# Kernel optimization log

Hardware: AMD Instinct MI355X
Metric: run time of the kernel (lower is better)

## Reference

```python
import jax, jax.numpy as jnp
import numpy as np

_EPS = 1e-06


def setup_inputs() -> dict:
    key = jax.random.key(0)
    k1, k2, k3, k4, k5 = jax.random.split(key, 5)
    B, N = 2, 8192
    return {
        "kp_before": jax.random.normal(k1, (B, N, 3), dtype=jnp.float32),
        "kp_warped_pred": jax.random.normal(k2, (B, N, 3), dtype=jnp.float32),
        "pose_gt": jax.random.normal(k3, (B, 3, 4), dtype=jnp.float32),
        "overlap_weights": jax.random.uniform(k4, (B, N), dtype=jnp.float32),
        "inlier_logits": jax.random.normal(k5, (B, N), dtype=jnp.float32),
    }


def _bce_with_logits(x, z):
    # elementwise BCEWithLogits: z*softplus(-x) + (1-z)*softplus(x)
    return z * jax.nn.softplus(-x) + (1.0 - z) * jax.nn.softplus(x)


def _balanced_loss(logits, label):
    # BalancedLoss: mean BCE within each of the 2 label groups, averaged over groups
    bce = _bce_with_logits(logits, label)
    loss = jnp.float32(0.0)
    for i in range(2):
        mask = (label == i).astype(jnp.float32)
        cnt = jnp.sum(mask)
        group = jnp.where(cnt > 0, jnp.sum(bce * mask) / jnp.maximum(cnt, 1.0), 0.0)
        loss = loss + group / 2.0
    return loss


def reference(kp_before, kp_warped_pred, pose_gt, overlap_weights, inlier_logits):
    B, N, _ = kp_before.shape
    M = B * N
    # se3_transform_list: warped_gt[b] = kp_before[b] @ R[b]^T + t[b]
    R = pose_gt[:, :, :3]            # [B,3,3]
    t = pose_gt[:, :, 3]             # [B,3]
    kp_warped_gt = jnp.einsum('bij,bnj->bni', R, kp_before) + t[:, None, :]
    # torch.cat(list, dim=0) over equal-sized chunks == reshape
    pred = kp_warped_pred.reshape(M, 3)
    gt = kp_warped_gt.reshape(M, 3)
    corr_err = pred - gt               # [M,3]
    # pairwise L2 distance matrix [M,M] (O(N^2) traffic) + 1-NN argmin
    sq = (jnp.sum(pred * pred, axis=1)[:, None]
          + jnp.sum(gt * gt, axis=1)[None, :]
          - 2.0 * (pred @ gt.T))
    dist_map = jnp.sqrt(jnp.maximum(sq, 0.0))
    knn_ind = jnp.argmin(dist_map, axis=1)
    binary_mask = (knn_ind == jnp.arange(M)).astype(jnp.float32)
    inlier_err = _balanced_loss(inlier_logits.reshape(M), binary_mask)
    # metric == 'mae'
    err = jnp.sum(jnp.abs(corr_err), axis=-1)  # [M]
    w = overlap_weights.reshape(M)
    mean_err = jnp.sum(w * err) / jnp.maximum(jnp.sum(w), _EPS)
    return mean_err + inlier_err
```

## Files before the change

### kernel.cpp

```cpp
#include <hip/hip_runtime.h>
#include <cstdint>

#define TPB 256
#define K_PRE 256
#define NSLICE 16

__global__ void __launch_bounds__(TPB) fused_prep_prefix(
        const float* __restrict__ kp_before,
        const float* __restrict__ pred,
        const float* __restrict__ pose,
        float4* __restrict__ gt4,
        float* __restrict__ thr,
        unsigned int* __restrict__ good,
        float* __restrict__ accum,
        int M, int N) {
    __shared__ float4 shg[K_PRE];
    int tid = threadIdx.x;
    int i = blockIdx.x * TPB + tid;

    if (blockIdx.x == 0 && tid < 8) accum[tid] = 0.0f;

    float sp = 0.f, tp0 = 0.f, tp1 = 0.f, tp2 = 0.f, dii = 0.f;
    if (i < M) {
        int b = i / N;
        const float* P = pose + b * 12;
        float k0 = kp_before[3*i+0];
        float k1 = kp_before[3*i+1];
        float k2 = kp_before[3*i+2];
        float g0 = fmaf(P[2],  k2, fmaf(P[1], k1, P[0]*k0)) + P[3];
        float g1 = fmaf(P[6],  k2, fmaf(P[5], k1, P[4]*k0)) + P[7];
        float g2 = fmaf(P[10], k2, fmaf(P[9], k1, P[8]*k0)) + P[11];
        float sg;
        {
            #pragma clang fp contract(off)
            sg = (g0*g0 + g1*g1) + g2*g2;
        }
        gt4[i] = make_float4(g0, g1, g2, sg);

        float p0 = pred[3*i+0], p1 = pred[3*i+1], p2 = pred[3*i+2];
        {
            #pragma clang fp contract(off)
            sp = (p0*p0 + p1*p1) + p2*p2;
        }
        tp0 = 2.0f*p0; tp1 = 2.0f*p1; tp2 = 2.0f*p2;
        float dot2 = fmaf(tp2, g2, fmaf(tp1, g1, tp0*g0));
        float v = (sp + sg) - dot2;
        dii = fmaxf(v, 0.0f);
        thr[i] = dii;
    }

    if (tid < K_PRE && tid < M) {
        int jp = tid;
        const float* Pj = pose + (jp / N) * 12;
        float q0 = kp_before[3*jp+0];
        float q1 = kp_before[3*jp+1];
        float q2 = kp_before[3*jp+2];
        float h0 = fmaf(Pj[2],  q2, fmaf(Pj[1], q1, Pj[0]*q0)) + Pj[3];
        float h1 = fmaf(Pj[6],  q2, fmaf(Pj[5], q1, Pj[4]*q0)) + Pj[7];
        float h2 = fmaf(Pj[10], q2, fmaf(Pj[9], q1, Pj[8]*q0)) + Pj[11];
        float hh;
        {
            #pragma clang fp contract(off)
            hh = (h0*h0 + h1*h1) + h2*h2;
        }
        shg[jp] = make_float4(h0, h1, h2, hh);
    }
    __syncthreads();

    if (i >= M) return;

    bool bad;
    if (i >= K_PRE) {
        float mn = __uint_as_float(0x7f7fffffu);
        for (int j = 0; j < K_PRE; j++) {
            float4 g = shg[j];
            float v = (sp + g.w) -
                      fmaf(tp2, g.z, fmaf(tp1, g.y, tp0 * g.x));
            mn = fminf(mn, v);
        }
        bad = (fmaxf(mn, 0.0f) <= dii);
    } else {
        float mnl = __uint_as_float(0x7f7fffffu);
        float mnr = __uint_as_float(0x7f7fffffu);
        for (int j = 0; j < i; j++) {
            float4 g = shg[j];
            float v = (sp + g.w) -
                      fmaf(tp2, g.z, fmaf(tp1, g.y, tp0 * g.x));
            mnl = fminf(mnl, v);
        }
        for (int j = i + 1; j < K_PRE; j++) {
            float4 g = shg[j];
            float v = (sp + g.w) -
                      fmaf(tp2, g.z, fmaf(tp1, g.y, tp0 * g.x));
            mnr = fminf(mnr, v);
        }
        bad = (fmaxf(mnl, 0.0f) <= dii) || (fmaxf(mnr, 0.0f) < dii);
    }
    good[i] = bad ? 0u : 1u;
}

__global__ void __launch_bounds__(TPB) suffix_kernel(
        const float* __restrict__ pred,
        const float4* __restrict__ gt4,
        const float* __restrict__ thr,
        unsigned int* __restrict__ good,
        int M) {
    __shared__ int cands[TPB];
    __shared__ int ncand;
    int s  = blockIdx.x & (NSLICE - 1);
    int r0 = (blockIdx.x / NSLICE) * TPB;
    if (threadIdx.x == 0) ncand = 0;
    __syncthreads();
    int i = r0 + threadIdx.x;
    if (i < M && good[i] == 1u) {
        int p = atomicAdd(&ncand, 1);
        cands[p] = i;
    }
    __syncthreads();
    int nc = ncand;
    if (nc == 0) return;

    int total = M - K_PRE;
    int per = (total + NSLICE - 1) / NSLICE;
    int js = K_PRE + s * per;
    int je = js + per; if (je > M) je = M;

    for (int e = 0; e < nc; e++) {
        int r = cands[e];
        float p0 = pred[3*r+0], p1 = pred[3*r+1], p2 = pred[3*r+2];
        float sp;
        {
            #pragma clang fp contract(off)
            sp = (p0*p0 + p1*p1) + p2*p2;
        }
        float tp0 = 2.0f*p0, tp1 = 2.0f*p1, tp2 = 2.0f*p2;
        float dii = thr[r];
        bool h = false;
        for (int j = js + threadIdx.x; j < je; j += TPB) {
            float4 g = gt4[j];
            float v = (sp + g.w) -
                      fmaf(tp2, g.z, fmaf(tp1, g.y, tp0 * g.x));
            float c = fmaxf(v, 0.0f);
            h = h || (c < dii && j != r) || (c == dii && j < r);
        }
        if (h) good[r] = 0u;
    }
}

__device__ inline float wave_red(float v) {
    #pragma unroll
    for (int off = 32; off > 0; off >>= 1) v += __shfl_down(v, off, 64);
    return v;
}

__global__ void __launch_bounds__(TPB) finalize_kernel(
        const float* __restrict__ pred,
        const float4* __restrict__ gt4,
        const float* __restrict__ ow,
        const float* __restrict__ logits,
        const unsigned int* __restrict__ good,
        float* __restrict__ accum,
        float* __restrict__ out,
        int M) {
    float werr = 0.f, wsum = 0.f, b1 = 0.f, c1 = 0.f, b0 = 0.f, c0 = 0.f;
    int stride = gridDim.x * blockDim.x;
    for (int i = blockIdx.x * blockDim.x + threadIdx.x; i < M; i += stride) {
        float x = logits[i];
        float l1p = log1pf(expf(-fabsf(x)));
        if (good[i] == 1u) {
            b1 += fmaxf(-x, 0.f) + l1p; c1 += 1.f;
        } else {
            b0 += fmaxf(x, 0.f) + l1p;  c0 += 1.f;
        }
        float4 g = gt4[i];
        float p0 = pred[3*i+0], p1 = pred[3*i+1], p2 = pred[3*i+2];
        float e = (fabsf(p0 - g.x) + fabsf(p1 - g.y)) + fabsf(p2 - g.z);
        float wi = ow[i];
        werr += wi * e;
        wsum += wi;
    }
    werr = wave_red(werr); wsum = wave_red(wsum);
    b1 = wave_red(b1); c1 = wave_red(c1);
    b0 = wave_red(b0); c0 = wave_red(c0);
    if ((threadIdx.x & 63) == 0) {
        atomicAdd(&accum[0], werr);
        atomicAdd(&accum[1], wsum);
        atomicAdd(&accum[2], b1);
        atomicAdd(&accum[3], c1);
        atomicAdd(&accum[4], b0);
        atomicAdd(&accum[5], c0);
    }
    __threadfence();
    __syncthreads();
    if (threadIdx.x == 0) {
        unsigned int* ctr = (unsigned int*)&accum[7];
        unsigned int old = atomicAdd(ctr, 1u);
        if (old == gridDim.x - 1) {
            float a0 = atomicAdd(&accum[0], 0.f);
            float a1 = atomicAdd(&accum[1], 0.f);
            float a2 = atomicAdd(&accum[2], 0.f);
            float a3 = atomicAdd(&accum[3], 0.f);
            float a4 = atomicAdd(&accum[4], 0.f);
            float a5 = atomicAdd(&accum[5], 0.f);
            float mean_err = a0 / fmaxf(a1, 1e-6f);
            float g1v = (a3 > 0.f) ? (a2 / fmaxf(a3, 1.f)) : 0.f;
            float g0v = (a5 > 0.f) ? (a4 / fmaxf(a5, 1.f)) : 0.f;
            out[0] = mean_err + (g0v * 0.5f + g1v * 0.5f);
        }
    }
}

extern "C" void kernel_launch(void* const* d_in, const int* in_sizes, int n_in,
                              void* d_out, int out_size, void* d_ws, size_t ws_size,
                              hipStream_t stream) {
    const float* kp_before = (const float*)d_in[0];
    const float* pred      = (const float*)d_in[1];
    const float* pose      = (const float*)d_in[2];
    const float* ow        = (const float*)d_in[3];
    const float* logits    = (const float*)d_in[4];
    float* out = (float*)d_out;

    int M = in_sizes[3];
    int B = in_sizes[2] / 12;
    int N = M / B;

    char* ws = (char*)d_ws;
    float4* gt4 = (float4*)ws;
    float* thr = (float*)(ws + (size_t)M * 16);
    unsigned int* good = (unsigned int*)(ws + (size_t)M * 20);
    float* accum = (float*)(ws + (size_t)M * 24);

    int nrb = (M + TPB - 1) / TPB;

    hipLaunchKernelGGL(fused_prep_prefix, dim3(nrb), dim3(TPB), 0, stream,
                       kp_before, pred, pose, gt4, thr, good, accum, M, N);

    hipLaunchKernelGGL(suffix_kernel, dim3(nrb * NSLICE), dim3(TPB), 0, stream,
                       pred, gt4, thr, good, M);

    hipLaunchKernelGGL(finalize_kernel, dim3(64), dim3(TPB), 0, stream,
                       pred, gt4, ow, logits, good, accum, out, M);
}
```

Measured before the change: 115.4 us.

## Prefilter against both batch prefixes and fuse suffix resolve with finalize

The shared-memory prefilter now checks each row against the first 256 gt points of both batch halves instead of only the first 256 overall, which is meant to reject more non-nearest candidates early. The separate sliced suffix kernel and the finalize kernel are merged. Each block now resolves its own surviving candidates by scanning the remaining columns itself and then reduces the loss terms directly. This saves one launch and the global good-array rewrite, but the per-candidate scan is no longer split across 16 slices, so blocks with many candidates do serial full-length scans and parallelism may drop.

```diff
diff --git a/kernel.cpp b/kernel.cpp
--- a/kernel.cpp
+++ b/kernel.cpp
@@ -2,8 +2,7 @@
 #include <cstdint>
 
 #define TPB 256
-#define K_PRE 256
-#define NSLICE 16
+#define PRE_PB 256
 
 __global__ void __launch_bounds__(TPB) fused_prep_prefix(
         const float* __restrict__ kp_before,
@@ -14,7 +13,7 @@
         unsigned int* __restrict__ good,
         float* __restrict__ accum,
         int M, int N) {
-    __shared__ float4 shg[K_PRE];
+    __shared__ float4 shg[2 * PRE_PB];
     int tid = threadIdx.x;
     int i = blockIdx.x * TPB + tid;
 
@@ -49,8 +48,10 @@
         thr[i] = dii;
     }
 
-    if (tid < K_PRE && tid < M) {
-        int jp = tid;
+    #pragma unroll
+    for (int half = 0; half < 2; half++) {
+        int jp = (half == 0) ? tid : (N + tid);
+        if (jp >= M) jp = tid;
         const float* Pj = pose + (jp / N) * 12;
         float q0 = kp_before[3*jp+0];
         float q1 = kp_before[3*jp+1];
@@ -63,67 +64,86 @@
             #pragma clang fp contract(off)
             hh = (h0*h0 + h1*h1) + h2*h2;
         }
-        shg[jp] = make_float4(h0, h1, h2, hh);
+        shg[half * PRE_PB + tid] = make_float4(h0, h1, h2, hh);
     }
     __syncthreads();
 
     if (i >= M) return;
 
     bool bad;
-    if (i >= K_PRE) {
+    bool cleanB = (i >= PRE_PB) && (i < N);
+    bool cleanA = (i >= N + PRE_PB);
+    if (cleanA) {
         float mn = __uint_as_float(0x7f7fffffu);
-        for (int j = 0; j < K_PRE; j++) {
-            float4 g = shg[j];
+        for (int k = 0; k < 2 * PRE_PB; k++) {
+            float4 g = shg[k];
             float v = (sp + g.w) -
                       fmaf(tp2, g.z, fmaf(tp1, g.y, tp0 * g.x));
             mn = fminf(mn, v);
         }
         bad = (fmaxf(mn, 0.0f) <= dii);
-    } else {
+    } else if (cleanB) {
         float mnl = __uint_as_float(0x7f7fffffu);
         float mnr = __uint_as_float(0x7f7fffffu);
-        for (int j = 0; j < i; j++) {
-            float4 g = shg[j];
+        for (int k = 0; k < PRE_PB; k++) {
+            float4 g = shg[k];
             float v = (sp + g.w) -
                       fmaf(tp2, g.z, fmaf(tp1, g.y, tp0 * g.x));
             mnl = fminf(mnl, v);
         }
-        for (int j = i + 1; j < K_PRE; j++) {
-            float4 g = shg[j];
+        for (int k = PRE_PB; k < 2 * PRE_PB; k++) {
+            float4 g = shg[k];
             float v = (sp + g.w) -
                       fmaf(tp2, g.z, fmaf(tp1, g.y, tp0 * g.x));
             mnr = fminf(mnr, v);
         }
         bad = (fmaxf(mnl, 0.0f) <= dii) || (fmaxf(mnr, 0.0f) < dii);
+    } else {
+        bool h = false;
+        for (int k = 0; k < 2 * PRE_PB; k++) {
+            int j = (k < PRE_PB) ? k : (N + k - PRE_PB);
+            if (j >= M) j = k - PRE_PB;
+            float4 g = shg[k];
+            float v = (sp + g.w) -
+                      fmaf(tp2, g.z, fmaf(tp1, g.y, tp0 * g.x));
+            float c = fmaxf(v, 0.0f);
+            h = h || (c < dii && j != i) || (c == dii && j < i);
+        }
+        bad = h;
     }
     good[i] = bad ? 0u : 1u;
 }
 
-__global__ void __launch_bounds__(TPB) suffix_kernel(
+__device__ inline float wave_red(float v) {
+    #pragma unroll
+    for (int off = 32; off > 0; off >>= 1) v += __shfl_down(v, off, 64);
+    return v;
+}
+
+__global__ void __launch_bounds__(TPB) resolve_finalize(
         const float* __restrict__ pred,
         const float4* __restrict__ gt4,
         const float* __restrict__ thr,
-        unsigned int* __restrict__ good,
-        int M) {
+        const unsigned int* __restrict__ good,
+        const float* __restrict__ ow,
+        const float* __restrict__ logits,
+        float* __restrict__ accum,
+        float* __restrict__ out,
+        int M, int N) {
     __shared__ int cands[TPB];
     __shared__ int ncand;
-    int s  = blockIdx.x & (NSLICE - 1);
-    int r0 = (blockIdx.x / NSLICE) * TPB;
-    if (threadIdx.x == 0) ncand = 0;
-    __syncthreads();
-    int i = r0 + threadIdx.x;
-    if (i < M && good[i] == 1u) {
-        int p = atomicAdd(&ncand, 1);
-        cands[p] = i;
-    }
+    __shared__ unsigned char verd[TPB];
+    int tid = threadIdx.x;
+    int r0 = blockIdx.x * TPB;
+    int i = r0 + tid;
+
+    if (tid == 0) ncand = 0;
+    __syncthreads();
+    unsigned int gi = (i < M) ? good[i] : 0u;
+    verd[tid] = (unsigned char)gi;
+    if (i < M && gi) { int p = atomicAdd(&ncand, 1); cands[p] = i; }
     __syncthreads();
     int nc = ncand;
-    if (nc == 0) return;
-
-    int total = M - K_PRE;
-    int per = (total + NSLICE - 1) / NSLICE;
-    int js = K_PRE + s * per;
-    int je = js + per; if (je > M) je = M;
 
     for (int e = 0; e < nc; e++) {
         int r = cands[e];
@@ -136,53 +156,44 @@
         float tp0 = 2.0f*p0, tp1 = 2.0f*p1, tp2 = 2.0f*p2;
         float dii = thr[r];
         bool h = false;
-        for (int j = js + threadIdx.x; j < je; j += TPB) {
+        for (int j = PRE_PB + tid; j < N; j += TPB) {
             float4 g = gt4[j];
             float v = (sp + g.w) -
                       fmaf(tp2, g.z, fmaf(tp1, g.y, tp0 * g.x));
             float c = fmaxf(v, 0.0f);
             h = h || (c < dii && j != r) || (c == dii && j < r);
         }
-        if (h) good[r] = 0u;
-    }
-}
-
-__device__ inline float wave_red(float v) {
-    #pragma unroll
-    for (int off = 32; off > 0; off >>= 1) v += __shfl_down(v, off, 64);
-    return v;
-}
-
-__global__ void __launch_bounds__(TPB) finalize_kernel(
-        const float* __restrict__ pred,
-        const float4* __restrict__ gt4,
-        const float* __restrict__ ow,
-        const float* __restrict__ logits,
-        const unsigned int* __restrict__ good,
-        float* __restrict__ accum,
-        float* __restrict__ out,
-        int M) {
+        for (int j = N + PRE_PB + tid; j < M; j += TPB) {
+            float4 g = gt4[j];
+            float v = (sp + g.w) -
+                      fmaf(tp2, g.z, fmaf(tp1, g.y, tp0 * g.x));
+            float c = fmaxf(v, 0.0f);
+            h = h || (c < dii && j != r) || (c == dii && j < r);
+        }
+        if (h) verd[r - r0] = 0;
+    }
+    __syncthreads();
+
     float werr = 0.f, wsum = 0.f, b1 = 0.f, c1 = 0.f, b0 = 0.f, c0 = 0.f;
-    int stride = gridDim.x * blockDim.x;
-    for (int i = blockIdx.x * blockDim.x + threadIdx.x; i < M; i += stride) {
+    if (i < M) {
         float x = logits[i];
         float l1p = log1pf(expf(-fabsf(x)));
-        if (good[i] == 1u) {
-            b1 += fmaxf(-x, 0.f) + l1p; c1 += 1.f;
+        if (verd[tid]) {
+            b1 = fmaxf(-x, 0.f) + l1p; c1 = 1.f;
         } else {
-            b0 += fmaxf(x, 0.f) + l1p;  c0 += 1.f;
+            b0 = fmaxf(x, 0.f) + l1p;  c0 = 1.f;
         }
         float4 g = gt4[i];
         float p0 = pred[3*i+0], p1 = pred[3*i+1], p2 = pred[3*i+2];
         float e = (fabsf(p0 - g.x) + fabsf(p1 - g.y)) + fabsf(p2 - g.z);
         float wi = ow[i];
-        werr += wi * e;
-        wsum += wi;
+        werr = wi * e;
+        wsum = wi;
     }
     werr = wave_red(werr); wsum = wave_red(wsum);
     b1 = wave_red(b1); c1 = wave_red(c1);
     b0 = wave_red(b0); c0 = wave_red(c0);
-    if ((threadIdx.x & 63) == 0) {
+    if ((tid & 63) == 0) {
         atomicAdd(&accum[0], werr);
         atomicAdd(&accum[1], wsum);
         atomicAdd(&accum[2], b1);
@@ -192,7 +203,7 @@
     }
     __threadfence();
     __syncthreads();
-    if (threadIdx.x == 0) {
+    if (tid == 0) {
         unsigned int* ctr = (unsigned int*)&accum[7];
         unsigned int old = atomicAdd(ctr, 1u);
         if (old == gridDim.x - 1) {
@@ -235,9 +246,6 @@
     hipLaunchKernelGGL(fused_prep_prefix, dim3(nrb), dim3(TPB), 0, stream,
                        kp_before, pred, pose, gt4, thr, good, accum, M, N);
 
-    hipLaunchKernelGGL(suffix_kernel, dim3(nrb * NSLICE), dim3(TPB), 0, stream,
-                       pred, gt4, thr, good, M);
-
-    hipLaunchKernelGGL(finalize_kernel, dim3(64), dim3(TPB), 0, stream,
-                       pred, gt4, ow, logits, good, accum, out, M);
-}
+    hipLaunchKernelGGL(resolve_finalize, dim3(nrb), dim3(TPB), 0, stream,
+                       pred, gt4, thr, good, ow, logits, accum, out, M, N);
+}
```

Result: slower. 161.3 us (+39.7%).
